# Performance work log

Hardware: AMD Instinct MI355X
Metric: run time of the kernel (lower is better)

The kernel has to match this reference:

```python
import jax, jax.numpy as jnp
import numpy as np

HIDDEN = 2048
NUM_HEADS = 16
HEAD_DIM = HIDDEN // NUM_HEADS
ROPE_THETA = 10000.0


def rope_tables(T, dim, base):
    inv_freq = 1.0 / (base ** (jnp.arange(0, dim, 2, dtype=jnp.float32) / dim))
    t = jnp.arange(T, dtype=jnp.float32)
    freqs = jnp.outer(t, inv_freq)              # [T, dim/2]
    emb = jnp.concatenate([freqs, freqs], -1)   # [T, dim]
    return jnp.cos(emb), jnp.sin(emb)


def rotate_half(x):
    x1, x2 = jnp.split(x, 2, axis=-1)
    return jnp.concatenate([-x2, x1], axis=-1)


def setup_inputs() -> dict:
    key = jax.random.key(0)
    ks = jax.random.split(key, 5)
    B, T, C = 2, 2048, HIDDEN
    s = 1.0 / np.sqrt(C)
    return {
        "x": jax.random.normal(ks[0], (B, T, C), jnp.float32),
        "Wq": jax.random.normal(ks[1], (C, C), jnp.float32) * s,
        "Wk": jax.random.normal(ks[2], (C, C), jnp.float32) * s,
        "Wv": jax.random.normal(ks[3], (C, C), jnp.float32) * s,
        "Wo": jax.random.normal(ks[4], (C, C), jnp.float32) * s,
    }


def reference(x, Wq, Wk, Wv, Wo):
    B, T, C = x.shape
    H, D = NUM_HEADS, HEAD_DIM
    scale = D ** -0.5

    # projections (torch Linear: y = x @ W.T)
    q = (x @ Wq.T).reshape(B, T, H, D).transpose(0, 2, 1, 3)  # [B,H,T,D]
    k = (x @ Wk.T).reshape(B, T, H, D).transpose(0, 2, 1, 3)
    v = (x @ Wv.T).reshape(B, T, H, D).transpose(0, 2, 1, 3)

    cos, sin = rope_tables(T, D, ROPE_THETA)  # [T, D]
    cos = cos[None, None, :, :]
    sin = sin[None, None, :, :]
    q = q * cos + rotate_half(q) * sin
    k = k * cos + rotate_half(k) * sin

    scores = jnp.einsum("bhqd,bhkd->bhqk", q, k) * scale
    causal = jnp.tril(jnp.ones((T, T), dtype=bool))
    scores = jnp.where(causal, scores, -jnp.inf)
    probs = jax.nn.softmax(scores, axis=-1)
    out = jnp.einsum("bhqk,bhkd->bhqd", probs, v)
    out = out.transpose(0, 2, 1, 3).reshape(B, T, C)
    return out @ Wo.T
```

## Files before the change

### kernel.cpp

```cpp
#include <hip/hip_runtime.h>
#include <hip/hip_bf16.h>


typedef __attribute__((ext_vector_type(4))) float f32x4;
typedef __attribute__((ext_vector_type(8))) short s16x8;
typedef __attribute__((ext_vector_type(4))) short s16x4;

typedef void __attribute__((address_space(1))) gvoid;
typedef void __attribute__((address_space(3))) svoid;
#define ASYNC16(ldsp, gp) __builtin_amdgcn_global_load_lds((gvoid*)(gp), (svoid*)(ldsp), 16, 0, 0)

__device__ __forceinline__ float bf2f(short b) {
  unsigned u = ((unsigned)(unsigned short)b) << 16;
  float f; __builtin_memcpy(&f, &u, 4); return f;
}
__device__ __forceinline__ short f2bf(float f) {
  unsigned u; __builtin_memcpy(&u, &f, 4);
  u += 0x7FFFu + ((u >> 16) & 1u);
  return (short)(u >> 16);
}

__device__ __forceinline__ f32x4 mfma16(s16x8 a, s16x8 b, f32x4 c) {
  return __builtin_amdgcn_mfma_f32_16x16x32_bf16(a, b, c, 0, 0, 0);
}

__global__ __launch_bounds__(256)
void cvt_k(const float* __restrict__ in, short* __restrict__ out, int n4) {
  int i = blockIdx.x * 256 + threadIdx.x;
  if (i < n4) {
    f32x4 v = *(const f32x4*)&in[i * 4];
    s16x4 o;
#pragma unroll
    for (int e = 0; e < 4; e++) o[e] = f2bf(v[e]);
    *(s16x4*)&out[i * 4] = o;
  }
}

__global__ __launch_bounds__(256)
void cvt_w4_k(const float* __restrict__ w0, const float* __restrict__ w1,
              const float* __restrict__ w2, const float* __restrict__ w3,
              short* __restrict__ o0, short* __restrict__ o1,
              short* __restrict__ o2, short* __restrict__ o3) {
  int i = blockIdx.x * 256 + threadIdx.x;
  int sel = i >> 20, j = i & 1048575;
  const float* in = (sel == 0) ? w0 : (sel == 1) ? w1 : (sel == 2) ? w2 : w3;
  short* out = (sel == 0) ? o0 : (sel == 1) ? o1 : (sel == 2) ? o2 : o3;
  f32x4 v = *(const f32x4*)&in[j * 4];
  s16x4 o;
#pragma unroll
  for (int e = 0; e < 4; e++) o[e] = f2bf(v[e]);
  *(s16x4*)&out[j * 4] = o;
}

__global__ void rope_tables_k(float* __restrict__ cosT, float* __restrict__ sinT) {
  int t = blockIdx.x, j = threadIdx.x;
  float inv = exp2f(-(float)j * 0.20762050593046f);
  float a = (float)t * inv;
  cosT[t * 64 + j] = cosf(a);
  sinT[t * 64 + j] = sinf(a);
}

__global__ __launch_bounds__(256)
void rope_apply_k(short* __restrict__ q, short* __restrict__ kk,
                  const float* __restrict__ cosT, const float* __restrict__ sinT) {
  int gid = blockIdx.x * 256 + threadIdx.x;
  int jb = (gid & 7) * 8;
  int h  = (gid >> 3) & 15;
  int row = gid >> 7;
  int t = row & 2047;
  long base = (long)row * 2048 + h * 128 + jb;
  float cc[8], ss[8];
  *(f32x4*)&cc[0] = *(const f32x4*)&cosT[t * 64 + jb];
  *(f32x4*)&cc[4] = *(const f32x4*)&cosT[t * 64 + jb + 4];
  *(f32x4*)&ss[0] = *(const f32x4*)&sinT[t * 64 + jb];
  *(f32x4*)&ss[4] = *(const f32x4*)&sinT[t * 64 + jb + 4];

  {
    s16x8 lo = *(s16x8*)&q[base];
    s16x8 hi = *(s16x8*)&q[base + 64];
    s16x8 nlo, nhi;
#pragma unroll
    for (int e = 0; e < 8; e++) {
      float a = bf2f(lo[e]), b = bf2f(hi[e]);
      nlo[e] = f2bf(a * cc[e] - b * ss[e]);
      nhi[e] = f2bf(b * cc[e] + a * ss[e]);
    }
    *(s16x8*)&q[base] = nlo;
    *(s16x8*)&q[base + 64] = nhi;
  }
  {
    s16x8 lo = *(s16x8*)&kk[base];
    s16x8 hi = *(s16x8*)&kk[base + 64];
    s16x8 nlo, nhi;
#pragma unroll
    for (int e = 0; e < 8; e++) {
      float a = bf2f(lo[e]), b = bf2f(hi[e]);
      nlo[e] = f2bf(a * cc[e] - b * ss[e]);
      nhi[e] = f2bf(b * cc[e] + a * ss[e]);
    }
    *(s16x8*)&kk[base] = nlo;
    *(s16x8*)&kk[base + 64] = nhi;
  }
}

__device__ __forceinline__ void store_out(float* p, float v) { *p = v; }
__device__ __forceinline__ void store_out(short* p, float v) { *p = f2bf(v); }


#define STAGE_A(Abase, buf, h, t)                                              \
  { ASYNC16(&As[(buf)*16384 + (h)*8192 + lin0*8],                              \
            (Abase) + (long)(m0 + (h)*128 + r0) * K + (t)*64 + kk0);           \
    ASYNC16(&As[(buf)*16384 + (h)*8192 + lin1*8],                              \
            (Abase) + (long)(m0 + (h)*128 + r1) * K + (t)*64 + kk1); }
#define STAGE_B(Bbase, buf, h, t)                                              \
  { ASYNC16(&Bs[(buf)*16384 + (h)*8192 + lin0*8],                              \
            (Bbase) + (long)((h)*128 + r0) * K + (t)*64 + kk0);                \
    ASYNC16(&Bs[(buf)*16384 + (h)*8192 + lin1*8],                              \
            (Bbase) + (long)((h)*128 + r1) * K + (t)*64 + kk1); }
#define LDA(mi, ks) (*(const s16x8*)&As[p*16384 +                              \
    (wr*128 + (mi)*16 + lr)*64 + (((ks)*4 + lk) ^ (lr & 7))*8])
#define LDB(ni, ks) (*(const s16x8*)&Bs[p*16384 +                              \
    (wc*64 + (ni)*16 + lr)*64 + (((ks)*4 + lk) ^ (lr & 7))*8])

template <typename OutT>
__device__ __forceinline__ void gemm8_tile(const short* __restrict__ A,
                                           const short* __restrict__ B,
                                           OutT* __restrict__ Cmat,
                                           int n0, int K, int ldc,
                                           short* As, short* Bs) {
  const int tid = threadIdx.x;
  const int wid = tid >> 6, lane = tid & 63;
  const int lr = lane & 15, lk = lane >> 4;
  const int wr = wid >> 2, wc = wid & 3;
  const int m0 = blockIdx.y * 256;

  const int lin0 = wid * 128 + lane;
  const int lin1 = wid * 128 + 64 + lane;
  const int r0 = lin0 >> 3, r1 = lin1 >> 3;
  const int kk0 = ((lin0 & 7) ^ (r0 & 7)) * 8;
  const int kk1 = ((lin1 & 7) ^ (r1 & 7)) * 8;

  f32x4 acc[8][4] = {};
  const int NT = K >> 6;

  STAGE_A(A, 0, 0, 0); STAGE_A(A, 0, 1, 0);
  STAGE_B(B, 0, 0, 0); STAGE_B(B, 0, 1, 0);
  STAGE_A(A, 1, 0, 1);
  asm volatile("s_waitcnt vmcnt(2)" ::: "memory");
  __builtin_amdgcn_sched_barrier(0);
  __builtin_amdgcn_s_barrier();

  for (int t = 0; t < NT; ++t) {
    const int p = t & 1;
    const bool s1 = (t + 1 < NT), s2 = (t + 2 < NT);
    s16x8 af[8], b0, b1;
#pragma unroll
    for (int mi = 0; mi < 8; mi++) af[mi] = LDA(mi, 0);
    b0 = LDB(0, 0); b1 = LDB(1, 0);
    if (s1) STAGE_A(A, p ^ 1, 1, t + 1);
    __builtin_amdgcn_s_barrier();
    __builtin_amdgcn_s_setprio(1);
#pragma unroll
    for (int mi = 0; mi < 8; mi++) {
      acc[mi][0] = mfma16(af[mi], b0, acc[mi][0]);
      acc[mi][1] = mfma16(af[mi], b1, acc[mi][1]);
    }
    __builtin_amdgcn_s_setprio(0);
    __builtin_amdgcn_s_barrier();
    b0 = LDB(2, 0); b1 = LDB(3, 0);
    if (s1) STAGE_B(B, p ^ 1, 0, t + 1);
    __builtin_amdgcn_s_barrier();
    __builtin_amdgcn_s_setprio(1);
#pragma unroll
    for (int mi = 0; mi < 8; mi++) {
      acc[mi][2] = mfma16(af[mi], b0, acc[mi][2]);
      acc[mi][3] = mfma16(af[mi], b1, acc[mi][3]);
    }
    __builtin_amdgcn_s_setprio(0);
    __builtin_amdgcn_s_barrier();
#pragma unroll
    for (int mi = 0; mi < 8; mi++) af[mi] = LDA(mi, 1);
    b0 = LDB(0, 1); b1 = LDB(1, 1);
    if (s1) STAGE_B(B, p ^ 1, 1, t + 1);
    __builtin_amdgcn_s_barrier();
    __builtin_amdgcn_s_setprio(1);
#pragma unroll
    for (int mi = 0; mi < 8; mi++) {
      acc[mi][0] = mfma16(af[mi], b0, acc[mi][0]);
      acc[mi][1] = mfma16(af[mi], b1, acc[mi][1]);
    }
    __builtin_amdgcn_s_setprio(0);
    __builtin_amdgcn_s_barrier();
    b0 = LDB(2, 1); b1 = LDB(3, 1);
    if (s2) {
      STAGE_A(A, p, 0, t + 2);
      asm volatile("s_waitcnt vmcnt(2)" ::: "memory");
    } else {
      asm volatile("s_waitcnt vmcnt(0)" ::: "memory");
    }
    __builtin_amdgcn_sched_barrier(0);
    __builtin_amdgcn_s_barrier();
    __builtin_amdgcn_s_setprio(1);
#pragma unroll
    for (int mi = 0; mi < 8; mi++) {
      acc[mi][2] = mfma16(af[mi], b0, acc[mi][2]);
      acc[mi][3] = mfma16(af[mi], b1, acc[mi][3]);
    }
    __builtin_amdgcn_s_setprio(0);
    __builtin_amdgcn_s_barrier();
  }
#pragma unroll
  for (int mi = 0; mi < 8; mi++)
#pragma unroll
    for (int ni = 0; ni < 4; ni++)
#pragma unroll
      for (int r = 0; r < 4; r++) {
        int row = m0 + wr * 128 + mi * 16 + lk * 4 + r;
        int col = n0 + wc * 64 + ni * 16 + lr;
        store_out(&Cmat[(long)row * ldc + col], acc[mi][ni][r]);
      }
}

__global__ __launch_bounds__(512, 2)
void gemm8_qkv_k(const short* __restrict__ A,
                 const short* __restrict__ Bq, const short* __restrict__ Bk,
                 const short* __restrict__ Bv,
                 short* __restrict__ Cq, short* __restrict__ Ck,
                 short* __restrict__ Cv, int K) {
  __shared__ short As[2 * 16384];
  __shared__ short Bs[2 * 16384];
  int sel = blockIdx.x >> 3;
  int ncol = (blockIdx.x & 7) * 256;
  const short* B = (sel == 0) ? Bq : (sel == 1) ? Bk : Bv;
  short* C = (sel == 0) ? Cq : (sel == 1) ? Ck : Cv;
  gemm8_tile<short>(A, B + (long)ncol * K, C, ncol, K, 2048, As, Bs);
}

__global__ __launch_bounds__(512, 2)
void gemm8_out_k(const short* __restrict__ A, const short* __restrict__ B,
                 float* __restrict__ C, int K) {
  __shared__ short As[2 * 16384];
  __shared__ short Bs[2 * 16384];
  int ncol = blockIdx.x * 256;
  gemm8_tile<float>(A, B + (long)ncol * K, C, ncol, K, 2048, As, Bs);
}

__global__ __launch_bounds__(256)
void attn_k(const short* __restrict__ q, const short* __restrict__ k,
            const short* __restrict__ v, short* __restrict__ o) {
  __shared__ short Ks[2][64 * 128];
  __shared__ short Vt[128 * 72];
  __shared__ short Pl[4][16 * 72];
  const int tid = threadIdx.x;
  const int wave = tid >> 6, lane = tid & 63;
  const int lr = lane & 15, lq = lane >> 4;
  const int h = blockIdx.y, b = blockIdx.z;
  const long rowb = (long)b * 2048;
  const int hoff = h * 128;
  const float scale = 0.08838834764831845f;

  const int vr = (tid & 31) * 2;
  const int vcol = (tid >> 5) * 16;

  for (int pass = 0; pass < 2; pass++) {
    const int qt = pass ? (31 - blockIdx.x) : blockIdx.x;
    const int qbase = qt * 64;
    const int nt = qt + 1;

    s16x8 qf[4];
    {
      const short* qp = q + (rowb + qbase + wave * 16 + lr) * 2048 + hoff + lq * 8;
#pragma unroll
      for (int ks = 0; ks < 4; ks++) qf[ks] = *(const s16x8*)(qp + ks * 32);
    }
    f32x4 acc[8] = {};
    float mrun[4], lrun[4];
#pragma unroll
    for (int r = 0; r < 4; r++) { mrun[r] = -1e30f; lrun[r] = 0.f; }

    s16x8 vl[4];
    {
      const short* vp = v + (rowb + vr) * 2048 + hoff + vcol;
      vl[0] = *(const s16x8*)vp;       vl[1] = *(const s16x8*)(vp + 8);
      vl[2] = *(const s16x8*)(vp + 2048); vl[3] = *(const s16x8*)(vp + 2048 + 8);
    }
#pragma unroll
    for (int L = 0; L < 4; L++) {
      int ci = L * 256 + tid;
      int krow = ci >> 4, dslot = ci & 15;
      int col = (dslot ^ (krow & 7)) * 8;
      ASYNC16(&Ks[0][ci * 8], k + (rowb + krow) * 2048 + hoff + col);
    }
#pragma unroll
    for (int e = 0; e < 16; e++) {
      int col = vcol + e;
      unsigned pk = (unsigned)(unsigned short)vl[e >> 3][e & 7]
                  | ((unsigned)(unsigned short)vl[2 + (e >> 3)][e & 7] << 16);
      *(unsigned*)&Vt[col * 72 + vr] = pk;
    }
    __syncthreads();

    int cur = 0;
    for (int ti = 0; ti < nt; ti++) {
      const int kv0 = ti * 64;
      const bool pre = (ti + 1 < nt);
      s16x8 vn[4];
      if (pre) {
        const short* vp = v + (rowb + kv0 + 64 + vr) * 2048 + hoff + vcol;
        vn[0] = *(const s16x8*)vp;       vn[1] = *(const s16x8*)(vp + 8);
        vn[2] = *(const s16x8*)(vp + 2048); vn[3] = *(const s16x8*)(vp + 2048 + 8);
#pragma unroll
        for (int L = 0; L < 4; L++) {
          int ci = L * 256 + tid;
          int krow = ci >> 4, dslot = ci & 15;
          int col = (dslot ^ (krow & 7)) * 8;
          ASYNC16(&Ks[cur ^ 1][ci * 8], k + (rowb + kv0 + 64 + krow) * 2048 + hoff + col);
        }
      }
      f32x4 s[4] = {};
#pragma unroll
      for (int kvf = 0; kvf < 4; kvf++) {
        const int krow = kvf * 16 + lr;
#pragma unroll
        for (int ks = 0; ks < 4; ks++) {
          int doff = ks * 4 + lq;
          s16x8 kf = *(const s16x8*)&Ks[cur][krow * 128 + ((doff ^ (krow & 7)) * 8)];
          s[kvf] = mfma16(qf[ks], kf, s[kvf]);
        }
      }
#pragma unroll
      for (int kvf = 0; kvf < 4; kvf++)
#pragma unroll
        for (int r = 0; r < 4; r++) s[kvf][r] *= scale;
      if (ti == nt - 1) {
#pragma unroll
        for (int kvf = 0; kvf < 4; kvf++) {
          int kvc = kv0 + kvf * 16 + lr;
#pragma unroll
          for (int r = 0; r < 4; r++) {
            int qr = qbase + wave * 16 + lq * 4 + r;
            if (kvc > qr) s[kvf][r] = -3.0e38f;
          }
        }
      }
      float mt[4], rs[4];
#pragma unroll
      for (int r = 0; r < 4; r++)
        mt[r] = fmaxf(fmaxf(s[0][r], s[1][r]), fmaxf(s[2][r], s[3][r]));
#pragma unroll
      for (int d = 1; d < 16; d <<= 1)
#pragma unroll
        for (int r = 0; r < 4; r++) mt[r] = fmaxf(mt[r], __shfl_xor(mt[r], d));
      int need = 0;
#pragma unroll
      for (int r = 0; r < 4; r++) need |= (mt[r] > mrun[r] + 8.f);
      if (__any(need)) {
#pragma unroll
        for (int r = 0; r < 4; r++) {
          float mn = fmaxf(mrun[r], mt[r]);
          float sf = __expf(mrun[r] - mn);
          mrun[r] = mn;
          lrun[r] *= sf;
#pragma unroll
          for (int df = 0; df < 8; df++) acc[df][r] *= sf;
        }
      }
      short* pw = &Pl[wave][0];
#pragma unroll
      for (int r = 0; r < 4; r++) rs[r] = 0.f;
#pragma unroll
      for (int kvf = 0; kvf < 4; kvf++)
#pragma unroll
        for (int r = 0; r < 4; r++) {
          float p = __expf(s[kvf][r] - mrun[r]);
          rs[r] += p;
          pw[(lq * 4 + r) * 72 + kvf * 16 + lr] = f2bf(p);
        }
#pragma unroll
      for (int d = 1; d < 16; d <<= 1)
#pragma unroll
        for (int r = 0; r < 4; r++) rs[r] += __shfl_xor(rs[r], d);
#pragma unroll
      for (int r = 0; r < 4; r++) lrun[r] += rs[r];
      s16x8 pf0 = *(const s16x8*)&pw[lr * 72 + lq * 8];
      s16x8 pf1 = *(const s16x8*)&pw[lr * 72 + 32 + lq * 8];
#pragma unroll
      for (int df = 0; df < 8; df++) {
        s16x8 vf0 = *(const s16x8*)&Vt[(df * 16 + lr) * 72 + lq * 8];
        s16x8 vf1 = *(const s16x8*)&Vt[(df * 16 + lr) * 72 + 32 + lq * 8];
        acc[df] = mfma16(pf0, vf0, acc[df]);
        acc[df] = mfma16(pf1, vf1, acc[df]);
      }
      __syncthreads();
      if (pre) {
#pragma unroll
        for (int e = 0; e < 16; e++) {
          int col = vcol + e;
          unsigned pk = (unsigned)(unsigned short)vn[e >> 3][e & 7]
                      | ((unsigned)(unsigned short)vn[2 + (e >> 3)][e & 7] << 16);
          *(unsigned*)&Vt[col * 72 + vr] = pk;
        }
        __syncthreads();
      }
      cur ^= 1;
    }
#pragma unroll
    for (int r = 0; r < 4; r++) {
      float inv = 1.0f / lrun[r];
      long orow = rowb + qbase + wave * 16 + lq * 4 + r;
#pragma unroll
      for (int df = 0; df < 8; df++)
        o[orow * 2048 + hoff + df * 16 + lr] = f2bf(acc[df][r] * inv);
    }
  }
}

extern "C" void kernel_launch(void* const* d_in, const int* in_sizes, int n_in,
                              void* d_out, int out_size, void* d_ws, size_t ws_size,
                              hipStream_t stream) {
  const float* x  = (const float*)d_in[0];
  const float* Wq = (const float*)d_in[1];
  const float* Wk = (const float*)d_in[2];
  const float* Wv = (const float*)d_in[3];
  const float* Wo = (const float*)d_in[4];
  float* out = (float*)d_out;

  char* p = (char*)d_ws;
  short* xb  = (short*)p; p += 8388608L * 2;
  short* wqb = (short*)p; p += 4194304L * 2;
  short* wkb = (short*)p; p += 4194304L * 2;
  short* wvb = (short*)p; p += 4194304L * 2;
  short* wob = (short*)p; p += 4194304L * 2;
  short* qb  = (short*)p; p += 8388608L * 2;
  short* kb  = (short*)p; p += 8388608L * 2;
  short* vb  = (short*)p; p += 8388608L * 2;
  short* ab  = (short*)p; p += 8388608L * 2;
  float* cosT = (float*)p; p += 131072L * 4;
  float* sinT = (float*)p; p += 131072L * 4;

  cvt_k<<<8192, 256, 0, stream>>>(x, xb, 2097152);
  cvt_w4_k<<<16384, 256, 0, stream>>>(Wq, Wk, Wv, Wo, wqb, wkb, wvb, wob);
  rope_tables_k<<<2048, 64, 0, stream>>>(cosT, sinT);

  gemm8_qkv_k<<<dim3(24, 16), 512, 0, stream>>>(xb, wqb, wkb, wvb, qb, kb, vb, 2048);

  rope_apply_k<<<2048, 256, 0, stream>>>(qb, kb, cosT, sinT);

  attn_k<<<dim3(16, 16, 2), 256, 0, stream>>>(qb, kb, vb, ab);

  gemm8_out_k<<<dim3(8, 16), 512, 0, stream>>>(ab, wob, out, 2048);
}
```

Before: 434.1 us.

## Restructure GEMM staging into K-half chunks and use 256x128 tiles for out-proj

Rewrites both bf16 GEMM kernels so that each 64-wide K tile is staged as two 32-wide halves with a new XOR swizzle. Loads for the next halves are issued uniformly, with clamped indices instead of branches, and gated by explicit vmcnt/lgkmcnt waits. The output projection now uses 256x128 tiles, giving 256 blocks instead of 128 so more CUs are busy. Launch bounds drop to 1 block per CU and K is hardcoded, trading occupancy and generality for a simpler pipeline. The clamped tail iterations issue redundant loads.

```diff
diff --git a/kernel.cpp b/kernel.cpp
--- a/kernel.cpp
+++ b/kernel.cpp
@@ -9,6 +9,7 @@
 typedef void __attribute__((address_space(1))) gvoid;
 typedef void __attribute__((address_space(3))) svoid;
 #define ASYNC16(ldsp, gp) __builtin_amdgcn_global_load_lds((gvoid*)(gp), (svoid*)(ldsp), 16, 0, 0)
+#define VMW(N) asm volatile("s_waitcnt vmcnt(" #N ")" ::: "memory")
 
 __device__ __forceinline__ float bf2f(short b) {
   unsigned u = ((unsigned)(unsigned short)b) << 16;
@@ -103,62 +104,59 @@
   }
 }
 
-__device__ __forceinline__ void store_out(float* p, float v) { *p = v; }
-__device__ __forceinline__ void store_out(short* p, float v) { *p = f2bf(v); }
-
-
-#define STAGE_A(Abase, buf, h, t)                                              \
-  { ASYNC16(&As[(buf)*16384 + (h)*8192 + lin0*8],                              \
-            (Abase) + (long)(m0 + (h)*128 + r0) * K + (t)*64 + kk0);           \
-    ASYNC16(&As[(buf)*16384 + (h)*8192 + lin1*8],                              \
-            (Abase) + (long)(m0 + (h)*128 + r1) * K + (t)*64 + kk1); }
-#define STAGE_B(Bbase, buf, h, t)                                              \
-  { ASYNC16(&Bs[(buf)*16384 + (h)*8192 + lin0*8],                              \
-            (Bbase) + (long)((h)*128 + r0) * K + (t)*64 + kk0);                \
-    ASYNC16(&Bs[(buf)*16384 + (h)*8192 + lin1*8],                              \
-            (Bbase) + (long)((h)*128 + r1) * K + (t)*64 + kk1); }
-#define LDA(mi, ks) (*(const s16x8*)&As[p*16384 +                              \
-    (wr*128 + (mi)*16 + lr)*64 + (((ks)*4 + lk) ^ (lr & 7))*8])
-#define LDB(ni, ks) (*(const s16x8*)&Bs[p*16384 +                              \
-    (wc*64 + (ni)*16 + lr)*64 + (((ks)*4 + lk) ^ (lr & 7))*8])
-
-template <typename OutT>
-__device__ __forceinline__ void gemm8_tile(const short* __restrict__ A,
-                                           const short* __restrict__ B,
-                                           OutT* __restrict__ Cmat,
-                                           int n0, int K, int ldc,
-                                           short* As, short* Bs) {
+__global__ __launch_bounds__(512, 1)
+void gemm_qkv8_k(const short* __restrict__ A,
+                 const short* __restrict__ Bq, const short* __restrict__ Bk,
+                 const short* __restrict__ Bv,
+                 short* __restrict__ Cq, short* __restrict__ Ck,
+                 short* __restrict__ Cv) {
+  const int K = 2048, NT = 32;
+  __shared__ short As[32768];
+  __shared__ short Bs[32768];
   const int tid = threadIdx.x;
   const int wid = tid >> 6, lane = tid & 63;
   const int lr = lane & 15, lk = lane >> 4;
   const int wr = wid >> 2, wc = wid & 3;
+  const int sel = blockIdx.x >> 3;
+  const int n0 = (blockIdx.x & 7) * 256;
   const int m0 = blockIdx.y * 256;
-
-  const int lin0 = wid * 128 + lane;
-  const int lin1 = wid * 128 + 64 + lane;
-  const int r0 = lin0 >> 3, r1 = lin1 >> 3;
-  const int kk0 = ((lin0 & 7) ^ (r0 & 7)) * 8;
-  const int kk1 = ((lin1 & 7) ^ (r1 & 7)) * 8;
+  const short* B = (sel == 0) ? Bq : (sel == 1) ? Bk : Bv;
+  short* C = (sel == 0) ? Cq : (sel == 1) ? Ck : Cv;
+  const short* PA = A + (long)m0 * K;
+  const short* PB = B + (long)n0 * K;
+
+  const int srow = tid >> 2;
+  const int scol = (((tid & 3) ^ (srow & 3) ^ ((srow >> 2) & 3))) * 8;
+  const int gsw = ((lk ^ (lr & 3) ^ ((lr >> 2) & 3))) * 8;
 
   f32x4 acc[8][4] = {};
-  const int NT = K >> 6;
-
-  STAGE_A(A, 0, 0, 0); STAGE_A(A, 0, 1, 0);
-  STAGE_B(B, 0, 0, 0); STAGE_B(B, 0, 1, 0);
-  STAGE_A(A, 1, 0, 1);
-  asm volatile("s_waitcnt vmcnt(2)" ::: "memory");
+
+#define STG(buf, ks, tt)                                                       \
+  { const long kof = (long)(tt) * 64 + (ks) * 32 + scol;                       \
+    ASYNC16(&As[(buf)*16384 + (ks)*8192 + tid*8],        PA + (long)srow*K + kof);        \
+    ASYNC16(&As[(buf)*16384 + (ks)*8192 + 4096 + tid*8], PA + (long)(srow+128)*K + kof);  \
+    ASYNC16(&Bs[(buf)*16384 + (ks)*8192 + tid*8],        PB + (long)srow*K + kof);        \
+    ASYNC16(&Bs[(buf)*16384 + (ks)*8192 + 4096 + tid*8], PB + (long)(srow+128)*K + kof); }
+#define LDA1(buf, ks, mi) (*(const s16x8*)&As[(buf)*16384 + (ks)*8192 + (wr*128 + (mi)*16 + lr)*32 + gsw])
+#define LDB1(buf, ks, ni) (*(const s16x8*)&Bs[(buf)*16384 + (ks)*8192 + (wc*64 + (ni)*16 + lr)*32 + gsw])
+
+  STG(0, 0, 0); STG(0, 1, 0); STG(1, 0, 1);
+  VMW(8);
   __builtin_amdgcn_sched_barrier(0);
   __builtin_amdgcn_s_barrier();
 
   for (int t = 0; t < NT; ++t) {
     const int p = t & 1;
-    const bool s1 = (t + 1 < NT), s2 = (t + 2 < NT);
+    const int tc1 = (t + 1 < NT) ? t + 1 : NT - 1;
+    const int tc0 = (t + 2 < NT) ? t + 2 : NT - 1;
     s16x8 af[8], b0, b1;
 #pragma unroll
-    for (int mi = 0; mi < 8; mi++) af[mi] = LDA(mi, 0);
-    b0 = LDB(0, 0); b1 = LDB(1, 0);
-    if (s1) STAGE_A(A, p ^ 1, 1, t + 1);
-    __builtin_amdgcn_s_barrier();
+    for (int mi = 0; mi < 8; mi++) af[mi] = LDA1(p, 0, mi);
+    b0 = LDB1(p, 0, 0); b1 = LDB1(p, 0, 1);
+    STG(p ^ 1, 1, tc1);
+    __builtin_amdgcn_s_barrier();
+    asm volatile("s_waitcnt lgkmcnt(0)" ::: "memory");
+    __builtin_amdgcn_sched_barrier(0);
     __builtin_amdgcn_s_setprio(1);
 #pragma unroll
     for (int mi = 0; mi < 8; mi++) {
@@ -167,9 +165,10 @@
     }
     __builtin_amdgcn_s_setprio(0);
     __builtin_amdgcn_s_barrier();
-    b0 = LDB(2, 0); b1 = LDB(3, 0);
-    if (s1) STAGE_B(B, p ^ 1, 0, t + 1);
-    __builtin_amdgcn_s_barrier();
+    b0 = LDB1(p, 0, 2); b1 = LDB1(p, 0, 3);
+    __builtin_amdgcn_s_barrier();
+    asm volatile("s_waitcnt lgkmcnt(0)" ::: "memory");
+    __builtin_amdgcn_sched_barrier(0);
     __builtin_amdgcn_s_setprio(1);
 #pragma unroll
     for (int mi = 0; mi < 8; mi++) {
@@ -177,12 +176,16 @@
       acc[mi][3] = mfma16(af[mi], b1, acc[mi][3]);
     }
     __builtin_amdgcn_s_setprio(0);
-    __builtin_amdgcn_s_barrier();
-#pragma unroll
-    for (int mi = 0; mi < 8; mi++) af[mi] = LDA(mi, 1);
-    b0 = LDB(0, 1); b1 = LDB(1, 1);
-    if (s1) STAGE_B(B, p ^ 1, 1, t + 1);
-    __builtin_amdgcn_s_barrier();
+    VMW(8);
+    __builtin_amdgcn_sched_barrier(0);
+    __builtin_amdgcn_s_barrier();
+#pragma unroll
+    for (int mi = 0; mi < 8; mi++) af[mi] = LDA1(p, 1, mi);
+    b0 = LDB1(p, 1, 0); b1 = LDB1(p, 1, 1);
+    STG(p, 0, tc0);
+    __builtin_amdgcn_s_barrier();
+    asm volatile("s_waitcnt lgkmcnt(0)" ::: "memory");
+    __builtin_amdgcn_sched_barrier(0);
     __builtin_amdgcn_s_setprio(1);
 #pragma unroll
     for (int mi = 0; mi < 8; mi++) {
@@ -191,15 +194,10 @@
     }
     __builtin_amdgcn_s_setprio(0);
     __builtin_amdgcn_s_barrier();
-    b0 = LDB(2, 1); b1 = LDB(3, 1);
-    if (s2) {
-      STAGE_A(A, p, 0, t + 2);
-      asm volatile("s_waitcnt vmcnt(2)" ::: "memory");
-    } else {
-      asm volatile("s_waitcnt vmcnt(0)" ::: "memory");
-    }
-    __builtin_amdgcn_sched_barrier(0);
-    __builtin_amdgcn_s_barrier();
+    b0 = LDB1(p, 1, 2); b1 = LDB1(p, 1, 3);
+    __builtin_amdgcn_s_barrier();
+    asm volatile("s_waitcnt lgkmcnt(0)" ::: "memory");
+    __builtin_amdgcn_sched_barrier(0);
     __builtin_amdgcn_s_setprio(1);
 #pragma unroll
     for (int mi = 0; mi < 8; mi++) {
@@ -207,8 +205,11 @@
       acc[mi][3] = mfma16(af[mi], b1, acc[mi][3]);
     }
     __builtin_amdgcn_s_setprio(0);
+    VMW(8);
+    __builtin_amdgcn_sched_barrier(0);
     __builtin_amdgcn_s_barrier();
   }
+  VMW(0);
 #pragma unroll
   for (int mi = 0; mi < 8; mi++)
 #pragma unroll
@@ -217,32 +218,101 @@
       for (int r = 0; r < 4; r++) {
         int row = m0 + wr * 128 + mi * 16 + lk * 4 + r;
         int col = n0 + wc * 64 + ni * 16 + lr;
-        store_out(&Cmat[(long)row * ldc + col], acc[mi][ni][r]);
-      }
-}
-
-__global__ __launch_bounds__(512, 2)
-void gemm8_qkv_k(const short* __restrict__ A,
-                 const short* __restrict__ Bq, const short* __restrict__ Bk,
-                 const short* __restrict__ Bv,
-                 short* __restrict__ Cq, short* __restrict__ Ck,
-                 short* __restrict__ Cv, int K) {
-  __shared__ short As[2 * 16384];
-  __shared__ short Bs[2 * 16384];
-  int sel = blockIdx.x >> 3;
-  int ncol = (blockIdx.x & 7) * 256;
-  const short* B = (sel == 0) ? Bq : (sel == 1) ? Bk : Bv;
-  short* C = (sel == 0) ? Cq : (sel == 1) ? Ck : Cv;
-  gemm8_tile<short>(A, B + (long)ncol * K, C, ncol, K, 2048, As, Bs);
-}
-
-__global__ __launch_bounds__(512, 2)
-void gemm8_out_k(const short* __restrict__ A, const short* __restrict__ B,
-                 float* __restrict__ C, int K) {
-  __shared__ short As[2 * 16384];
-  __shared__ short Bs[2 * 16384];
-  int ncol = blockIdx.x * 256;
-  gemm8_tile<float>(A, B + (long)ncol * K, C, ncol, K, 2048, As, Bs);
+        C[(long)row * 2048 + col] = f2bf(acc[mi][ni][r]);
+      }
+#undef STG
+#undef LDA1
+#undef LDB1
+}
+
+__global__ __launch_bounds__(512, 1)
+void gemm_out8_k(const short* __restrict__ A, const short* __restrict__ Bw,
+                 float* __restrict__ C) {
+  const int K = 2048, NT = 32;
+  __shared__ short As[32768];
+  __shared__ short Bs[16384];
+  const int tid = threadIdx.x;
+  const int wid = tid >> 6, lane = tid & 63;
+  const int lr = lane & 15, lk = lane >> 4;
+  const int wr = wid >> 2, wc = wid & 3;
+  const int n0 = blockIdx.x * 128;
+  const int m0 = blockIdx.y * 256;
+  const short* PA = A + (long)m0 * K;
+  const short* PB = Bw + (long)n0 * K;
+
+  const int srow = tid >> 2;
+  const int scol = (((tid & 3) ^ (srow & 3) ^ ((srow >> 2) & 3))) * 8;
+  const int gsw = ((lk ^ (lr & 3) ^ ((lr >> 2) & 3))) * 8;
+
+  f32x4 acc[8][2] = {};
+
+#define STGO(buf, ks, tt)                                                      \
+  { const long kof = (long)(tt) * 64 + (ks) * 32 + scol;                       \
+    ASYNC16(&As[(buf)*16384 + (ks)*8192 + tid*8],        PA + (long)srow*K + kof);        \
+    ASYNC16(&As[(buf)*16384 + (ks)*8192 + 4096 + tid*8], PA + (long)(srow+128)*K + kof);  \
+    ASYNC16(&Bs[(buf)*8192 + (ks)*4096 + tid*8],         PB + (long)srow*K + kof); }
+#define LDAO(buf, ks, mi) (*(const s16x8*)&As[(buf)*16384 + (ks)*8192 + (wr*128 + (mi)*16 + lr)*32 + gsw])
+#define LDBO(buf, ks, ni) (*(const s16x8*)&Bs[(buf)*8192 + (ks)*4096 + (wc*32 + (ni)*16 + lr)*32 + gsw])
+
+  STGO(0, 0, 0); STGO(0, 1, 0); STGO(1, 0, 1);
+  VMW(6);
+  __builtin_amdgcn_sched_barrier(0);
+  __builtin_amdgcn_s_barrier();
+
+  for (int t = 0; t < NT; ++t) {
+    const int p = t & 1;
+    const int tc1 = (t + 1 < NT) ? t + 1 : NT - 1;
+    const int tc0 = (t + 2 < NT) ? t + 2 : NT - 1;
+    s16x8 af[8], b0, b1;
+#pragma unroll
+    for (int mi = 0; mi < 8; mi++) af[mi] = LDAO(p, 0, mi);
+    b0 = LDBO(p, 0, 0); b1 = LDBO(p, 0, 1);
+    STGO(p ^ 1, 1, tc1);
+    __builtin_amdgcn_s_barrier();
+    asm volatile("s_waitcnt lgkmcnt(0)" ::: "memory");
+    __builtin_amdgcn_sched_barrier(0);
+    __builtin_amdgcn_s_setprio(1);
+#pragma unroll
+    for (int mi = 0; mi < 8; mi++) {
+      acc[mi][0] = mfma16(af[mi], b0, acc[mi][0]);
+      acc[mi][1] = mfma16(af[mi], b1, acc[mi][1]);
+    }
+    __builtin_amdgcn_s_setprio(0);
+    VMW(6);
+    __builtin_amdgcn_sched_barrier(0);
+    __builtin_amdgcn_s_barrier();
+#pragma unroll
+    for (int mi = 0; mi < 8; mi++) af[mi] = LDAO(p, 1, mi);
+    b0 = LDBO(p, 1, 0); b1 = LDBO(p, 1, 1);
+    STGO(p, 0, tc0);
+    __builtin_amdgcn_s_barrier();
+    asm volatile("s_waitcnt lgkmcnt(0)" ::: "memory");
+    __builtin_amdgcn_sched_barrier(0);
+    __builtin_amdgcn_s_setprio(1);
+#pragma unroll
+    for (int mi = 0; mi < 8; mi++) {
+      acc[mi][0] = mfma16(af[mi], b0, acc[mi][0]);
+      acc[mi][1] = mfma16(af[mi], b1, acc[mi][1]);
+    }
+    __builtin_amdgcn_s_setprio(0);
+    VMW(6);
+    __builtin_amdgcn_sched_barrier(0);
+    __builtin_amdgcn_s_barrier();
+  }
+  VMW(0);
+#pragma unroll
+  for (int mi = 0; mi < 8; mi++)
+#pragma unroll
+    for (int ni = 0; ni < 2; ni++)
+#pragma unroll
+      for (int r = 0; r < 4; r++) {
+        int row = m0 + wr * 128 + mi * 16 + lk * 4 + r;
+        int col = n0 + wc * 32 + ni * 16 + lr;
+        C[(long)row * 2048 + col] = acc[mi][ni][r];
+      }
+#undef STGO
+#undef LDAO
+#undef LDBO
 }
 
 __global__ __launch_bounds__(256)
@@ -442,11 +512,11 @@
   cvt_w4_k<<<16384, 256, 0, stream>>>(Wq, Wk, Wv, Wo, wqb, wkb, wvb, wob);
   rope_tables_k<<<2048, 64, 0, stream>>>(cosT, sinT);
 
-  gemm8_qkv_k<<<dim3(24, 16), 512, 0, stream>>>(xb, wqb, wkb, wvb, qb, kb, vb, 2048);
+  gemm_qkv8_k<<<dim3(24, 16), 512, 0, stream>>>(xb, wqb, wkb, wvb, qb, kb, vb);
 
   rope_apply_k<<<2048, 256, 0, stream>>>(qb, kb, cosT, sinT);
 
   attn_k<<<dim3(16, 16, 2), 256, 0, stream>>>(qb, kb, vb, ab);
 
-  gemm8_out_k<<<dim3(8, 16), 512, 0, stream>>>(ab, wob, out, 2048);
-}
+  gemm_out8_k<<<dim3(16, 16), 512, 0, stream>>>(ab, wob, out);
+}
```

Measured after the change: 427.5 us. Within noise of the previous version (-1.5%).
